# Performance work log

Measured on AMD Instinct MI355X. Metric: run time of the kernel, lower is better.

Reference implementation:

```python
import jax, jax.numpy as jnp
import numpy as np

COMBS = ((0, 1), (0, 2), (1, 2))
OUT_DIM, TIME_RANK, RANK = 3, 4, 4


def grid_sample_nd(grid, coords):
    """Multilinear interpolation. grid: [C, *R] (d spatial dims), coords: [N, d] in [-1, 1].
    align_corners=True, border clamp. Returns [N, C]."""
    d = coords.shape[-1]
    i0s, ws = [], []
    for k in range(d):
        R = grid.shape[1 + k]
        x = jnp.clip((coords[:, k] + 1.0) * 0.5 * (R - 1), 0.0, R - 1)
        i0 = jnp.clip(jnp.floor(x).astype(jnp.int32), 0, R - 2)
        i0s.append(i0)
        ws.append(x - i0)
    out = jnp.zeros((grid.shape[0], coords.shape[0]), grid.dtype)
    for corner in range(2 ** d):
        idx, w = [], jnp.ones((coords.shape[0],), grid.dtype)
        for k in range(d):
            b = (corner >> k) & 1
            idx.append(i0s[k] + b)
            w = w * (ws[k] if b else 1.0 - ws[k])
        out = out + grid[(slice(None),) + tuple(idx)] * w  # [C, N]
    return out.T


def setup_inputs():
    key = jax.random.key(0)
    ks = jax.random.split(key, 16)
    n_rays, S = 4096, 128
    N = n_rays * S
    R, T, F = 128, 150, 32
    rays_d = jax.random.normal(ks[0], (n_rays, 3), jnp.float32)
    pts = jax.random.uniform(ks[1], (N, 3), jnp.float32, -1.0, 1.0)
    times = jax.random.uniform(ks[2], (N,), jnp.float32, -1.0, 1.0)
    deltas = jax.random.uniform(ks[3], (N,), jnp.float32) * 0.02 + 1e-3
    ridx = jnp.repeat(jnp.arange(n_rays, dtype=jnp.int32), S)
    boundary = (jnp.arange(N) % S) == 0
    bg_color = jax.random.uniform(ks[4], (n_rays, 3), jnp.float32)
    grid_space = jax.random.normal(ks[5], (3, RANK * OUT_DIM * TIME_RANK, R, R), jnp.float32) * 0.1
    grid_time = jax.random.normal(ks[6], (OUT_DIM * TIME_RANK, T), jnp.float32) * 0.1
    features = jax.random.normal(ks[7], (F, R, R, R), jnp.float32) * 0.1
    W1 = jax.random.normal(ks[8], (F + 3, 64), jnp.float32) * 0.05
    b1 = jnp.zeros((64,), jnp.float32)
    W2 = jax.random.normal(ks[9], (64, 16), jnp.float32) * 0.05
    b2 = jnp.zeros((16,), jnp.float32)
    Wc1 = jax.random.normal(ks[10], (15 + 3, 64), jnp.float32) * 0.05
    bc1 = jnp.zeros((64,), jnp.float32)
    Wc2 = jax.random.normal(ks[11], (64, 3), jnp.float32) * 0.05
    bc2 = jnp.zeros((3,), jnp.float32)
    return {"rays_d": rays_d, "pts": pts, "times": times, "deltas": deltas,
            "bg_color": bg_color, "grid_space": grid_space, "grid_time": grid_time,
            "features": features, "W1": W1, "b1": b1, "W2": W2, "b2": b2,
            "Wc1": Wc1, "bc1": bc1, "Wc2": Wc2, "bc2": bc2,
            "ridx": ridx, "boundary": boundary}


def reference(rays_d, pts, times, deltas, bg_color, grid_space, grid_time, features,
              W1, b1, W2, b2, Wc1, bc1, Wc2, bc2, ridx, boundary):
    n_rays = rays_d.shape[0]
    N = pts.shape[0]
    rays_d = rays_d / jnp.linalg.norm(rays_d, axis=-1, keepdims=True)
    rd = rays_d[ridx]  # [N, 3] per-sample ray dirs

    # --- low-rank spatio-temporal feature coordinates ---
    it = grid_sample_nd(grid_time, times[:, None]).reshape(N, OUT_DIM, TIME_RANK)
    sp = jnp.stack([grid_sample_nd(grid_space[c], pts[:, list(comb)])
                    for c, comb in enumerate(COMBS)])  # [3, N, rank*out*tr]
    sp = sp.reshape(3, N, OUT_DIM, TIME_RANK, RANK)
    sp = jnp.prod(sp, axis=0).sum(axis=-1)            # [N, out_dim, time_rank]
    coords = jnp.clip((sp * it).sum(axis=-1), -1.0, 1.0)  # [N, 3]
    feats = grid_sample_nd(features, coords)          # [N, F]

    # --- MLP decoder (sigma + color) ---
    h = jax.nn.relu(jnp.concatenate([feats, rd], axis=-1) @ W1 + b1)
    s = h @ W2 + b2
    sigma = jnp.exp(jnp.clip(s[:, 0], -15.0, 15.0))   # trunc_exp
    geo = s[:, 1:]
    hc = jax.nn.relu(jnp.concatenate([geo, rd], axis=-1) @ Wc1 + bc1)
    rgb = jax.nn.sigmoid(hc @ Wc2 + bc2)              # [N, 3]

    # --- segment volumetric integration (exclusive transmittance) ---
    tau = sigma * deltas
    excl = jnp.cumsum(tau) - tau
    bmask = boundary.astype(tau.dtype)
    seg_first = jax.ops.segment_sum(excl * bmask, ridx, num_segments=n_rays)
    Tr = jnp.exp(-(excl - seg_first[ridx]))
    w = Tr * (1.0 - jnp.exp(-tau))                    # per-sample weights
    ray_colors = jax.ops.segment_sum(w[:, None] * rgb, ridx, num_segments=n_rays)
    alpha = jax.ops.segment_sum(w, ridx, num_segments=n_rays)
    return ray_colors + (1.0 - alpha)[:, None] * bg_color
```

## Files before the change

kernel.cpp:

```cpp
#include <hip/hip_runtime.h>
#include <hip/hip_fp16.h>
#include <math.h>

#define RR 128
#define TT 150
#define NCH 48
#define NF 32

typedef float vf2 __attribute__((ext_vector_type(2)));
typedef unsigned int u4v __attribute__((ext_vector_type(4)));
typedef _Float16 h2 __attribute__((ext_vector_type(2)));
typedef _Float16 h4 __attribute__((ext_vector_type(4)));
typedef float fv4 __attribute__((ext_vector_type(4)));

__device__ __forceinline__ h2 pack2(float a, float b) {
    h2 r; r[0] = (_Float16)a; r[1] = (_Float16)b; return r;
}
__device__ __forceinline__ void up4p(uint u, vf2 s, vf2* a) {
    a[0] += __builtin_amdgcn_cvt_pk_f32_fp8(u, false) * s;
    a[1] += __builtin_amdgcn_cvt_pk_f32_fp8(u, true) * s;
}
__device__ __forceinline__ void up16p(u4v q, float sf, vf2* a) {
    vf2 s; s[0] = sf; s[1] = sf;
    up4p(q[0], s, a + 0); up4p(q[1], s, a + 2);
    up4p(q[2], s, a + 4); up4p(q[3], s, a + 6);
}

__global__ __launch_bounds__(256) void tgsp_8(const float* __restrict__ in,
                                              uint* __restrict__ out) {
    __shared__ float lds[48][65];
    const int t = threadIdx.x;
    const int p = blockIdx.x >> 8;
    const int tile = blockIdx.x & 255;
    const size_t V = (size_t)RR * RR;
    const size_t v0 = (size_t)tile * 64;
    const float* ip = in + (size_t)p * NCH * V;
    uint* op = out + (size_t)p * V * 12;
    #pragma unroll
    for (int k = 0; k < 12; k++) {
        int idx = k * 256 + t; int c = idx >> 6; int vv = idx & 63;
        lds[c][vv] = ip[(size_t)c * V + v0 + vv];
    }
    __syncthreads();
    #pragma unroll
    for (int k = 0; k < 3; k++) {
        int idx = k * 256 + t; int vv = idx / 12; int cp = idx - vv * 12;
        float a = lds[4 * cp + 0][vv] * 128.f;
        float b = lds[4 * cp + 1][vv] * 128.f;
        float c = lds[4 * cp + 2][vv] * 128.f;
        float d = lds[4 * cp + 3][vv] * 128.f;
        uint w = (uint)__builtin_amdgcn_cvt_pk_fp8_f32(a, b, 0, false);
        w = (uint)__builtin_amdgcn_cvt_pk_fp8_f32(c, d, w, true);
        op[(v0 + vv) * 12 + cp] = w;
    }
}

template<bool TR>
__global__ __launch_bounds__(256, 4) void lrv_main(
    const float* __restrict__ rays_d,
    const float* __restrict__ pts,
    const float* __restrict__ times,
    const float* __restrict__ deltas,
    const float* __restrict__ bg,
    const void* __restrict__ gspace_p,
    const float* __restrict__ gtime,
    const float* __restrict__ feat,
    const float* __restrict__ W1, const float* __restrict__ b1,
    const float* __restrict__ W2, const float* __restrict__ b2,
    const float* __restrict__ Wc1, const float* __restrict__ bc1,
    const float* __restrict__ Wc2, const float* __restrict__ bc2,
    const int*  __restrict__ ridx,
    float* __restrict__ out)
{
    __shared__ __align__(16) _Float16 sW1t[64 * 48];
    __shared__ __align__(16) _Float16 sW2t[16 * 68];
    __shared__ __align__(16) _Float16 sWc1t[64 * 36];
    __shared__ __align__(16) _Float16 sWc2t[16 * 68];
    __shared__ __align__(16) _Float16 sX[4 * 64 * 48];
    __shared__ float sb1[64], sbc1[64], sb2[16], sbc2[4];
    __shared__ int sV[4], sU[4];
    __shared__ float waveTot[4];
    __shared__ float4 rbuf[4];
    float4 (*sFeatV)[8] = reinterpret_cast<float4(*)[8]>(sX);

    const int tid  = threadIdx.x;
    const int lane = tid & 63;
    const int wv   = tid >> 6;
    const int lg   = lane >> 4;
    const int ll   = lane & 15;

    {
        for (int k = tid; k < 64 * 48; k += 256) {
            int n = k / 48, kk = k - n * 48;
            sW1t[k] = (_Float16)((kk < 35) ? W1[kk * 64 + n] : 0.f);
        }
        for (int k = tid; k < 16 * 68; k += 256) {
            int o = k / 68, n = k - o * 68;
            sW2t[k] = (_Float16)((n < 64) ? W2[n * 16 + o] : 0.f);
        }
        for (int k = tid; k < 64 * 36; k += 256) {
            int n = k / 36, kk = k - n * 36;
            sWc1t[k] = (_Float16)((kk < 18) ? Wc1[kk * 64 + n] : 0.f);
        }
        for (int k = tid; k < 16 * 68; k += 256) {
            int o = k / 68, n = k - o * 68;
            sWc2t[k] = (_Float16)((o < 3 && n < 64) ? Wc2[n * 3 + o] : 0.f);
        }
        if (tid < 64) { sb1[tid] = b1[tid]; sbc1[tid] = bc1[tid]; }
        if (tid < 16) sb2[tid] = b2[tid];
        if (tid < 3)  sbc2[tid] = bc2[tid];
    }
    __syncthreads();

    const int ray = blockIdx.x * 2 + (tid >> 7);
    const int i   = ray * 128 + (tid & 127);

    float itv[12];
    {
        float t = times[i];
        float x = (t + 1.f) * 0.5f * (float)(TT - 1);
        x = fminf(fmaxf(x, 0.f), (float)(TT - 1));
        int ti0 = (int)floorf(x);
        ti0 = min(max(ti0, 0), TT - 2);
        float tw = x - (float)ti0;
        #pragma unroll
        for (int c = 0; c < 12; c++) {
            float v0 = gtime[c * TT + ti0];
            float v1 = gtime[c * TT + ti0 + 1];
            itv[c] = fmaf(tw, v1 - v0, v0);
        }
    }

    float p0 = pts[i * 3 + 0], p1 = pts[i * 3 + 1], p2 = pts[i * 3 + 2];
    int   pbia[3], pbib[3];
    float pw[3][4];
    {
        const float pa[3] = { p0, p0, p1 };
        const float pb[3] = { p1, p2, p2 };
        #pragma unroll
        for (int c = 0; c < 3; c++) {
            float xa = fminf(fmaxf((pa[c] + 1.f) * 0.5f * (float)(RR - 1), 0.f), (float)(RR - 1));
            float xb = fminf(fmaxf((pb[c] + 1.f) * 0.5f * (float)(RR - 1), 0.f), (float)(RR - 1));
            int ia = min(max((int)floorf(xa), 0), RR - 2);
            int ib = min(max((int)floorf(xb), 0), RR - 2);
            float wa = xa - (float)ia, wb = xb - (float)ib;
            pbia[c] = ia; pbib[c] = ib;
            pw[c][0] = (1.f - wa) * (1.f - wb);
            pw[c][1] = (1.f - wa) * wb;
            pw[c][2] = wa * (1.f - wb);
            pw[c][3] = wa * wb;
        }
    }
    float S12[12];
    if constexpr (TR) {
        const uint* gs = (const uint*)gspace_p;
        uint b[3][4];
        #pragma unroll
        for (int c = 0; c < 3; c++) {
            uint b00 = ((uint)c * (RR * RR) + (uint)pbia[c] * RR + (uint)pbib[c]) * 12u;
            b[c][0] = b00;            b[c][1] = b00 + 12u;
            b[c][2] = b00 + RR * 12u; b[c][3] = b00 + RR * 12u + 12u;
        }
        #pragma unroll
        for (int cb = 0; cb < 3; cb++) {
            vf2 pr[8];
            #pragma unroll
            for (int p = 0; p < 3; p++) {
                vf2 a[8];
                #pragma unroll
                for (int j = 0; j < 8; j++) { a[j][0] = 0.f; a[j][1] = 0.f; }
                #pragma unroll
                for (int corner = 0; corner < 4; corner++) {
                    u4v q = *reinterpret_cast<const u4v*>(gs + b[p][corner] + cb * 4);
                    up16p(q, pw[p][corner] * 0.0078125f, a);
                }
                #pragma unroll
                for (int j = 0; j < 8; j++) pr[j] = (p == 0) ? a[j] : pr[j] * a[j];
            }
            #pragma unroll
            for (int g = 0; g < 4; g++)
                S12[cb * 4 + g] = pr[2 * g][0] + pr[2 * g][1]
                                + pr[2 * g + 1][0] + pr[2 * g + 1][1];
        }
    } else {
        const float* gs = (const float*)gspace_p;
        #pragma unroll
        for (int k = 0; k < 12; k++) S12[k] = 0.f;
        #pragma unroll 4
        for (int ch = 0; ch < NCH; ch++) {
            float prod = 1.f;
            #pragma unroll
            for (int c = 0; c < 3; c++) {
                const float* g = gs + (size_t)(c * NCH + ch) * (RR * RR)
                               + pbia[c] * RR + pbib[c];
                float v = pw[c][0] * g[0] + pw[c][1] * g[1]
                        + pw[c][2] * g[RR] + pw[c][3] * g[RR + 1];
                prod *= v;
            }
            S12[ch >> 2] += prod;
        }
    }
    float cc[3];
    #pragma unroll
    for (int o = 0; o < 3; o++) {
        float a = 0.f;
        #pragma unroll
        for (int t = 0; t < 4; t++) a += S12[o * 4 + t] * itv[o * 4 + t];
        cc[o] = fminf(fmaxf(a, -1.f), 1.f);
    }

    __align__(16) float in35[36];
    int   fi[3];
    float cw[8];
    {
        float fw[3];
        #pragma unroll
        for (int k = 0; k < 3; k++) {
            float xk = fminf(fmaxf((cc[k] + 1.f) * 0.5f * (float)(RR - 1), 0.f), (float)(RR - 1));
            int ik = min(max((int)floorf(xk), 0), RR - 2);
            fi[k] = ik; fw[k] = xk - (float)ik;
        }
        float w0 = fw[0], w1 = fw[1], w2 = fw[2];
        cw[0] = (1.f - w0) * (1.f - w1) * (1.f - w2);
        cw[1] = (1.f - w0) * (1.f - w1) * w2;
        cw[2] = (1.f - w0) * w1 * (1.f - w2);
        cw[3] = (1.f - w0) * w1 * w2;
        cw[4] = w0 * (1.f - w1) * (1.f - w2);
        cw[5] = w0 * (1.f - w1) * w2;
        cw[6] = w0 * w1 * (1.f - w2);
        cw[7] = w0 * w1 * w2;
    }
    {
        int packed = (fi[0] << 16) | (fi[1] << 8) | fi[2];
        int first  = __builtin_amdgcn_readfirstlane(packed);
        unsigned long long bal = __ballot(packed == first);
        if (lane == 0) { sV[wv] = first; sU[wv] = (bal == ~0ull) ? 1 : 0; }
    }
    __syncthreads();
    const bool uni = sU[0] && sU[1] && sU[2] && sU[3] &&
                     sV[0] == sV[1] && sV[1] == sV[2] && sV[2] == sV[3];
    const size_t V3 = (size_t)RR * RR * RR;
    if (uni) {
        {
            int c  = tid >> 5;
            int ch = tid & 31;
            size_t off = (((size_t)(fi[0] + ((c >> 2) & 1)) * RR
                         + (size_t)(fi[1] + ((c >> 1) & 1))) * RR
                         + (size_t)(fi[2] + (c & 1)));
            ((float*)sFeatV)[c * 32 + ch] = feat[(size_t)ch * V3 + off];
        }
        __syncthreads();
        float4* in4 = reinterpret_cast<float4*>(in35);
        #pragma unroll
        for (int chq = 0; chq < 8; chq++) {
            float4 acc = make_float4(0.f, 0.f, 0.f, 0.f);
            #pragma unroll
            for (int c = 0; c < 8; c++) {
                float4 v = sFeatV[c][chq];
                acc.x = fmaf(cw[c], v.x, acc.x);
                acc.y = fmaf(cw[c], v.y, acc.y);
                acc.z = fmaf(cw[c], v.z, acc.z);
                acc.w = fmaf(cw[c], v.w, acc.w);
            }
            in4[chq] = acc;
        }
    } else {
        size_t fb = ((size_t)fi[0] * RR + fi[1]) * RR + fi[2];
        #pragma unroll 4
        for (int ch = 0; ch < NF; ch++) {
            const float* f = feat + (size_t)ch * V3 + fb;
            in35[ch] = cw[0] * f[0]            + cw[1] * f[1]
                     + cw[2] * f[RR]           + cw[3] * f[RR + 1]
                     + cw[4] * f[RR * RR]      + cw[5] * f[RR * RR + 1]
                     + cw[6] * f[RR * RR + RR] + cw[7] * f[RR * RR + RR + 1];
        }
    }
    {
        int r = ridx[i];
        float d0 = rays_d[r * 3 + 0], d1 = rays_d[r * 3 + 1], d2 = rays_d[r * 3 + 2];
        float inv = 1.f / sqrtf(d0 * d0 + d1 * d1 + d2 * d2);
        in35[32] = d0 * inv; in35[33] = d1 * inv; in35[34] = d2 * inv;
    }
    __syncthreads();

    _Float16* Xw = sX + wv * (64 * 48);
    float* Srow  = (float*)Xw;

    {
        u4v xw[6];
        #pragma unroll
        for (int t6 = 0; t6 < 6; t6++) {
            #pragma unroll
            for (int e = 0; e < 4; e++) {
                int q = t6 * 4 + e;
                float a = (2 * q     < 35) ? in35[2 * q]     : 0.f;
                float b = (2 * q + 1 < 35) ? in35[2 * q + 1] : 0.f;
                xw[t6][e] = __builtin_bit_cast(uint, pack2(a, b));
            }
        }
        u4v* xrow = (u4v*)(Xw + lane * 48);
        #pragma unroll
        for (int t6 = 0; t6 < 6; t6++) xrow[t6] = xw[t6];
    }

    fv4 bb[4];
    #pragma unroll
    for (int hr = 0; hr < 4; hr++)
        bb[hr] = *(const fv4*)&sb1[hr * 16 + (lg << 2)];
    fv4 b2v = *(const fv4*)&sb2[lg << 2];

    #pragma unroll
    for (int half = 0; half < 2; half++) {
        fv4 acc1[4][2];
        #pragma unroll
        for (int hr = 0; hr < 4; hr++) {
            acc1[hr][0] = bb[hr];
            acc1[hr][1] = bb[hr];
        }
        #pragma unroll
        for (int ks = 0; ks < 3; ks++) {
            h4 a1[4], b1f[2];
            #pragma unroll
            for (int hr = 0; hr < 4; hr++)
                a1[hr] = *(const h4*)&sW1t[(hr * 16 + ll) * 48 + ks * 16 + (lg << 2)];
            #pragma unroll
            for (int s2 = 0; s2 < 2; s2++) {
                int sc = half * 2 + s2;
                b1f[s2] = *(const h4*)&Xw[(sc * 16 + ll) * 48 + ks * 16 + (lg << 2)];
            }
            #pragma unroll
            for (int hr = 0; hr < 4; hr++) {
                acc1[hr][0] = __builtin_amdgcn_mfma_f32_16x16x16f16(a1[hr], b1f[0], acc1[hr][0], 0, 0, 0);
                acc1[hr][1] = __builtin_amdgcn_mfma_f32_16x16x16f16(a1[hr], b1f[1], acc1[hr][1], 0, 0, 0);
            }
        }
        #pragma unroll
        for (int s2 = 0; s2 < 2; s2++) {
            fv4 acc2 = b2v;
            #pragma unroll
            for (int ks = 0; ks < 4; ks++) {
                fv4 g = acc1[ks][s2];
                h4 hb;
                #pragma unroll
                for (int e = 0; e < 4; e++) hb[e] = (_Float16)fmaxf(g[e], 0.f);
                h4 a2 = *(const h4*)&sW2t[ll * 68 + ks * 16 + (lg << 2)];
                acc2 = __builtin_amdgcn_mfma_f32_16x16x16f16(a2, hb, acc2, 0, 0, 0);
            }
            int sc = half * 2 + s2;
            *(fv4*)&Srow[(sc * 16 + ll) * 20 + (lg << 2)] = acc2;
        }
    }

    float sacc[16];
    #pragma unroll
    for (int q = 0; q < 4; q++) {
        fv4 v = *(const fv4*)&Srow[lane * 20 + q * 4];
        sacc[q * 4 + 0] = v[0]; sacc[q * 4 + 1] = v[1];
        sacc[q * 4 + 2] = v[2]; sacc[q * 4 + 3] = v[3];
    }
    float sigma = __expf(fminf(fmaxf(sacc[0], -15.f), 15.f));

    {
        float xi[18];
        #pragma unroll
        for (int k = 0; k < 15; k++) xi[k] = sacc[k + 1];
        xi[15] = in35[32]; xi[16] = in35[33]; xi[17] = in35[34];
        uint wd[16];
        #pragma unroll
        for (int q = 0; q < 9; q++)
            wd[q] = __builtin_bit_cast(uint, pack2(xi[2 * q], (2 * q + 1 < 18) ? xi[2 * q + 1] : 0.f));
        #pragma unroll
        for (int q = 9; q < 16; q++) wd[q] = 0u;
        u4v* xrow = (u4v*)(Xw + lane * 48);
        #pragma unroll
        for (int t4 = 0; t4 < 4; t4++) {
            u4v v; v[0] = wd[t4 * 4 + 0]; v[1] = wd[t4 * 4 + 1];
                   v[2] = wd[t4 * 4 + 2]; v[3] = wd[t4 * 4 + 3];
            xrow[t4] = v;
        }
    }
    fv4 bbc[4];
    #pragma unroll
    for (int hr = 0; hr < 4; hr++)
        bbc[hr] = *(const fv4*)&sbc1[hr * 16 + (lg << 2)];
    fv4 c2bias;
    c2bias[0] = (lg == 0) ? sbc2[0] : 0.f;
    c2bias[1] = (lg == 0) ? sbc2[1] : 0.f;
    c2bias[2] = (lg == 0) ? sbc2[2] : 0.f;
    c2bias[3] = 0.f;

    float rc0 = 0.f, rc1 = 0.f, rc2 = 0.f;
    #pragma unroll
    for (int sc = 0; sc < 4; sc++) {
        fv4 acc1c[4];
        #pragma unroll
        for (int hr = 0; hr < 4; hr++) acc1c[hr] = bbc[hr];
        #pragma unroll
        for (int ks = 0; ks < 2; ks++) {
            h4 bfrag = *(const h4*)&Xw[(sc * 16 + ll) * 48 + ks * 16 + (lg << 2)];
            #pragma unroll
            for (int hr = 0; hr < 4; hr++) {
                h4 a = *(const h4*)&sWc1t[(hr * 16 + ll) * 36 + ks * 16 + (lg << 2)];
                acc1c[hr] = __builtin_amdgcn_mfma_f32_16x16x16f16(a, bfrag, acc1c[hr], 0, 0, 0);
            }
        }
        fv4 acc2c = c2bias;
        #pragma unroll
        for (int ks = 0; ks < 4; ks++) {
            fv4 g = acc1c[ks];
            h4 hb;
            #pragma unroll
            for (int e = 0; e < 4; e++) hb[e] = (_Float16)fmaxf(g[e], 0.f);
            h4 a2 = *(const h4*)&sWc2t[ll * 68 + ks * 16 + (lg << 2)];
            acc2c = __builtin_amdgcn_mfma_f32_16x16x16f16(a2, hb, acc2c, 0, 0, 0);
        }
        float t0 = __shfl(acc2c[0], ll, 64);
        float t1 = __shfl(acc2c[1], ll, 64);
        float t2 = __shfl(acc2c[2], ll, 64);
        if (lg == sc) { rc0 = t0; rc1 = t1; rc2 = t2; }
    }
    float r_ = 1.f / (1.f + __expf(-rc0));
    float g_ = 1.f / (1.f + __expf(-rc1));
    float b_ = 1.f / (1.f + __expf(-rc2));

    float tau = sigma * deltas[i];
    float v = tau;
    #pragma unroll
    for (int off = 1; off < 64; off <<= 1) {
        float u = __shfl_up(v, off, 64);
        if (lane >= off) v += u;
    }
    if (lane == 63) waveTot[wv] = v;
    float excl = v - tau;
    __syncthreads();
    if (wv & 1) excl += waveTot[wv & 2];

    float Tr = __expf(-excl);
    float w  = Tr * (1.f - __expf(-tau));

    float ax = w * r_, ay = w * g_, az = w * b_, aw = w;
    #pragma unroll
    for (int off = 32; off; off >>= 1) {
        ax += __shfl_down(ax, off, 64);
        ay += __shfl_down(ay, off, 64);
        az += __shfl_down(az, off, 64);
        aw += __shfl_down(aw, off, 64);
    }
    if (lane == 0) rbuf[wv] = make_float4(ax, ay, az, aw);
    __syncthreads();
    if (lane == 0 && (wv & 1) == 0) {
        float cx = rbuf[wv].x + rbuf[wv + 1].x;
        float cy = rbuf[wv].y + rbuf[wv + 1].y;
        float cz = rbuf[wv].z + rbuf[wv + 1].z;
        float alpha = rbuf[wv].w + rbuf[wv + 1].w;
        out[ray * 3 + 0] = cx + (1.f - alpha) * bg[ray * 3 + 0];
        out[ray * 3 + 1] = cy + (1.f - alpha) * bg[ray * 3 + 1];
        out[ray * 3 + 2] = cz + (1.f - alpha) * bg[ray * 3 + 2];
    }
}

extern "C" void kernel_launch(void* const* d_in, const int* in_sizes, int n_in,
                              void* d_out, int out_size, void* d_ws, size_t ws_size,
                              hipStream_t stream) {
    const float* rays_d = (const float*)d_in[0];
    const float* pts    = (const float*)d_in[1];
    const float* times  = (const float*)d_in[2];
    const float* deltas = (const float*)d_in[3];
    const float* bg     = (const float*)d_in[4];
    const float* gspace = (const float*)d_in[5];
    const float* gtime  = (const float*)d_in[6];
    const float* feat   = (const float*)d_in[7];
    const float* W1  = (const float*)d_in[8];
    const float* b1  = (const float*)d_in[9];
    const float* W2  = (const float*)d_in[10];
    const float* b2  = (const float*)d_in[11];
    const float* Wc1 = (const float*)d_in[12];
    const float* bc1 = (const float*)d_in[13];
    const float* Wc2 = (const float*)d_in[14];
    const float* bc2 = (const float*)d_in[15];
    const int*   ridx = (const int*)d_in[16];

    const int n_rays = in_sizes[0] / 3;

    const size_t GSP_8B = (size_t)3 * RR * RR * NCH;

    if (ws_size >= GSP_8B) {
        uint* gsp_t = (uint*)d_ws;
        tgsp_8<<<dim3(3 * 256), dim3(256), 0, stream>>>(gspace, gsp_t);
        lrv_main<true><<<dim3(n_rays / 2), dim3(256), 0, stream>>>(
            rays_d, pts, times, deltas, bg, (const void*)gsp_t, gtime, feat,
            W1, b1, W2, b2, Wc1, bc1, Wc2, bc2, ridx, (float*)d_out);
    } else {
        lrv_main<false><<<dim3(n_rays / 2), dim3(256), 0, stream>>>(
            rays_d, pts, times, deltas, bg, (const void*)gspace, gtime, feat,
            W1, b1, W2, b2, Wc1, bc1, Wc2, bc2, ridx, (float*)d_out);
    }
}
```

Baseline: 115.3 us.

## Halve per-wave MLP LDS staging via two-pass processing to raise occupancy

Shrinks the per-wave fp16 activation staging buffer from 64 to 32 rows. The MLP runs in two passes, with half the lanes writing their rows each pass. sFeatV gets its own small buffer instead of aliasing sX, and launch bounds rise to 5 blocks per CU. The goal is to fit more resident blocks by cutting LDS use, which hides gather latency better, at the cost of extra LDS round-trips and a tighter register budget that may cause spills.

```diff
diff --git a/kernel.cpp b/kernel.cpp
--- a/kernel.cpp
+++ b/kernel.cpp
@@ -56,7 +56,7 @@
 }
 
 template<bool TR>
-__global__ __launch_bounds__(256, 4) void lrv_main(
+__global__ __launch_bounds__(256, 5) void lrv_main(
     const float* __restrict__ rays_d,
     const float* __restrict__ pts,
     const float* __restrict__ times,
@@ -76,18 +76,20 @@
     __shared__ __align__(16) _Float16 sW2t[16 * 68];
     __shared__ __align__(16) _Float16 sWc1t[64 * 36];
     __shared__ __align__(16) _Float16 sWc2t[16 * 68];
-    __shared__ __align__(16) _Float16 sX[4 * 64 * 48];
+    __shared__ __align__(16) _Float16 sX[4 * 32 * 48];
+    __shared__ __align__(16) float4 sFeatV[8][8];
     __shared__ float sb1[64], sbc1[64], sb2[16], sbc2[4];
     __shared__ int sV[4], sU[4];
     __shared__ float waveTot[4];
     __shared__ float4 rbuf[4];
-    float4 (*sFeatV)[8] = reinterpret_cast<float4(*)[8]>(sX);
 
     const int tid  = threadIdx.x;
     const int lane = tid & 63;
     const int wv   = tid >> 6;
     const int lg   = lane >> 4;
     const int ll   = lane & 15;
+    const int myPass = lane >> 5;
+    const int mrow   = lane & 31;
 
     {
         for (int k = tid; k < 64 * 48; k += 256) {
@@ -281,27 +283,9 @@
         float inv = 1.f / sqrtf(d0 * d0 + d1 * d1 + d2 * d2);
         in35[32] = d0 * inv; in35[33] = d1 * inv; in35[34] = d2 * inv;
     }
-    __syncthreads();
-
-    _Float16* Xw = sX + wv * (64 * 48);
+
+    _Float16* Xw = sX + wv * (32 * 48);
     float* Srow  = (float*)Xw;
-
-    {
-        u4v xw[6];
-        #pragma unroll
-        for (int t6 = 0; t6 < 6; t6++) {
-            #pragma unroll
-            for (int e = 0; e < 4; e++) {
-                int q = t6 * 4 + e;
-                float a = (2 * q     < 35) ? in35[2 * q]     : 0.f;
-                float b = (2 * q + 1 < 35) ? in35[2 * q + 1] : 0.f;
-                xw[t6][e] = __builtin_bit_cast(uint, pack2(a, b));
-            }
-        }
-        u4v* xrow = (u4v*)(Xw + lane * 48);
-        #pragma unroll
-        for (int t6 = 0; t6 < 6; t6++) xrow[t6] = xw[t6];
-    }
 
     fv4 bb[4];
     #pragma unroll
@@ -309,14 +293,28 @@
         bb[hr] = *(const fv4*)&sb1[hr * 16 + (lg << 2)];
     fv4 b2v = *(const fv4*)&sb2[lg << 2];
 
-    #pragma unroll
-    for (int half = 0; half < 2; half++) {
+    float sacc[16];
+    #pragma unroll
+    for (int pass = 0; pass < 2; pass++) {
+        if (myPass == pass) {
+            u4v xw[6];
+            #pragma unroll
+            for (int t6 = 0; t6 < 6; t6++) {
+                #pragma unroll
+                for (int e = 0; e < 4; e++) {
+                    int q = t6 * 4 + e;
+                    float a = (2 * q     < 35) ? in35[2 * q]     : 0.f;
+                    float b = (2 * q + 1 < 35) ? in35[2 * q + 1] : 0.f;
+                    xw[t6][e] = __builtin_bit_cast(uint, pack2(a, b));
+                }
+            }
+            u4v* xrow = (u4v*)(Xw + mrow * 48);
+            #pragma unroll
+            for (int t6 = 0; t6 < 6; t6++) xrow[t6] = xw[t6];
+        }
         fv4 acc1[4][2];
         #pragma unroll
-        for (int hr = 0; hr < 4; hr++) {
-            acc1[hr][0] = bb[hr];
-            acc1[hr][1] = bb[hr];
-        }
+        for (int hr = 0; hr < 4; hr++) { acc1[hr][0] = bb[hr]; acc1[hr][1] = bb[hr]; }
         #pragma unroll
         for (int ks = 0; ks < 3; ks++) {
             h4 a1[4], b1f[2];
@@ -324,10 +322,8 @@
             for (int hr = 0; hr < 4; hr++)
                 a1[hr] = *(const h4*)&sW1t[(hr * 16 + ll) * 48 + ks * 16 + (lg << 2)];
             #pragma unroll
-            for (int s2 = 0; s2 < 2; s2++) {
-                int sc = half * 2 + s2;
-                b1f[s2] = *(const h4*)&Xw[(sc * 16 + ll) * 48 + ks * 16 + (lg << 2)];
-            }
+            for (int s2 = 0; s2 < 2; s2++)
+                b1f[s2] = *(const h4*)&Xw[(s2 * 16 + ll) * 48 + ks * 16 + (lg << 2)];
             #pragma unroll
             for (int hr = 0; hr < 4; hr++) {
                 acc1[hr][0] = __builtin_amdgcn_mfma_f32_16x16x16f16(a1[hr], b1f[0], acc1[hr][0], 0, 0, 0);
@@ -346,39 +342,19 @@
                 h4 a2 = *(const h4*)&sW2t[ll * 68 + ks * 16 + (lg << 2)];
                 acc2 = __builtin_amdgcn_mfma_f32_16x16x16f16(a2, hb, acc2, 0, 0, 0);
             }
-            int sc = half * 2 + s2;
-            *(fv4*)&Srow[(sc * 16 + ll) * 20 + (lg << 2)] = acc2;
-        }
-    }
-
-    float sacc[16];
-    #pragma unroll
-    for (int q = 0; q < 4; q++) {
-        fv4 v = *(const fv4*)&Srow[lane * 20 + q * 4];
-        sacc[q * 4 + 0] = v[0]; sacc[q * 4 + 1] = v[1];
-        sacc[q * 4 + 2] = v[2]; sacc[q * 4 + 3] = v[3];
+            *(fv4*)&Srow[(s2 * 16 + ll) * 20 + (lg << 2)] = acc2;
+        }
+        if (myPass == pass) {
+            #pragma unroll
+            for (int q = 0; q < 4; q++) {
+                fv4 v = *(const fv4*)&Srow[mrow * 20 + q * 4];
+                sacc[q * 4 + 0] = v[0]; sacc[q * 4 + 1] = v[1];
+                sacc[q * 4 + 2] = v[2]; sacc[q * 4 + 3] = v[3];
+            }
+        }
     }
     float sigma = __expf(fminf(fmaxf(sacc[0], -15.f), 15.f));
 
-    {
-        float xi[18];
-        #pragma unroll
-        for (int k = 0; k < 15; k++) xi[k] = sacc[k + 1];
-        xi[15] = in35[32]; xi[16] = in35[33]; xi[17] = in35[34];
-        uint wd[16];
-        #pragma unroll
-        for (int q = 0; q < 9; q++)
-            wd[q] = __builtin_bit_cast(uint, pack2(xi[2 * q], (2 * q + 1 < 18) ? xi[2 * q + 1] : 0.f));
-        #pragma unroll
-        for (int q = 9; q < 16; q++) wd[q] = 0u;
-        u4v* xrow = (u4v*)(Xw + lane * 48);
-        #pragma unroll
-        for (int t4 = 0; t4 < 4; t4++) {
-            u4v v; v[0] = wd[t4 * 4 + 0]; v[1] = wd[t4 * 4 + 1];
-                   v[2] = wd[t4 * 4 + 2]; v[3] = wd[t4 * 4 + 3];
-            xrow[t4] = v;
-        }
-    }
     fv4 bbc[4];
     #pragma unroll
     for (int hr = 0; hr < 4; hr++)
@@ -391,33 +367,55 @@
 
     float rc0 = 0.f, rc1 = 0.f, rc2 = 0.f;
     #pragma unroll
-    for (int sc = 0; sc < 4; sc++) {
-        fv4 acc1c[4];
-        #pragma unroll
-        for (int hr = 0; hr < 4; hr++) acc1c[hr] = bbc[hr];
-        #pragma unroll
-        for (int ks = 0; ks < 2; ks++) {
-            h4 bfrag = *(const h4*)&Xw[(sc * 16 + ll) * 48 + ks * 16 + (lg << 2)];
-            #pragma unroll
-            for (int hr = 0; hr < 4; hr++) {
-                h4 a = *(const h4*)&sWc1t[(hr * 16 + ll) * 36 + ks * 16 + (lg << 2)];
-                acc1c[hr] = __builtin_amdgcn_mfma_f32_16x16x16f16(a, bfrag, acc1c[hr], 0, 0, 0);
-            }
-        }
-        fv4 acc2c = c2bias;
-        #pragma unroll
-        for (int ks = 0; ks < 4; ks++) {
-            fv4 g = acc1c[ks];
-            h4 hb;
-            #pragma unroll
-            for (int e = 0; e < 4; e++) hb[e] = (_Float16)fmaxf(g[e], 0.f);
-            h4 a2 = *(const h4*)&sWc2t[ll * 68 + ks * 16 + (lg << 2)];
-            acc2c = __builtin_amdgcn_mfma_f32_16x16x16f16(a2, hb, acc2c, 0, 0, 0);
-        }
-        float t0 = __shfl(acc2c[0], ll, 64);
-        float t1 = __shfl(acc2c[1], ll, 64);
-        float t2 = __shfl(acc2c[2], ll, 64);
-        if (lg == sc) { rc0 = t0; rc1 = t1; rc2 = t2; }
+    for (int pass = 0; pass < 2; pass++) {
+        if (myPass == pass) {
+            float xi[18];
+            #pragma unroll
+            for (int k = 0; k < 15; k++) xi[k] = sacc[k + 1];
+            xi[15] = in35[32]; xi[16] = in35[33]; xi[17] = in35[34];
+            uint wd[16];
+            #pragma unroll
+            for (int q = 0; q < 9; q++)
+                wd[q] = __builtin_bit_cast(uint, pack2(xi[2 * q], (2 * q + 1 < 18) ? xi[2 * q + 1] : 0.f));
+            #pragma unroll
+            for (int q = 9; q < 16; q++) wd[q] = 0u;
+            u4v* xrow = (u4v*)(Xw + mrow * 48);
+            #pragma unroll
+            for (int t4 = 0; t4 < 4; t4++) {
+                u4v v; v[0] = wd[t4 * 4 + 0]; v[1] = wd[t4 * 4 + 1];
+                       v[2] = wd[t4 * 4 + 2]; v[3] = wd[t4 * 4 + 3];
+                xrow[t4] = v;
+            }
+        }
+        #pragma unroll
+        for (int scl = 0; scl < 2; scl++) {
+            fv4 acc1c[4];
+            #pragma unroll
+            for (int hr = 0; hr < 4; hr++) acc1c[hr] = bbc[hr];
+            #pragma unroll
+            for (int ks = 0; ks < 2; ks++) {
+                h4 bfrag = *(const h4*)&Xw[(scl * 16 + ll) * 48 + ks * 16 + (lg << 2)];
+                #pragma unroll
+                for (int hr = 0; hr < 4; hr++) {
+                    h4 a = *(const h4*)&sWc1t[(hr * 16 + ll) * 36 + ks * 16 + (lg << 2)];
+                    acc1c[hr] = __builtin_amdgcn_mfma_f32_16x16x16f16(a, bfrag, acc1c[hr], 0, 0, 0);
+                }
+            }
+            fv4 acc2c = c2bias;
+            #pragma unroll
+            for (int ks = 0; ks < 4; ks++) {
+                fv4 g = acc1c[ks];
+                h4 hb;
+                #pragma unroll
+                for (int e = 0; e < 4; e++) hb[e] = (_Float16)fmaxf(g[e], 0.f);
+                h4 a2 = *(const h4*)&sWc2t[ll * 68 + ks * 16 + (lg << 2)];
+                acc2c = __builtin_amdgcn_mfma_f32_16x16x16f16(a2, hb, acc2c, 0, 0, 0);
+            }
+            float t0 = __shfl(acc2c[0], ll, 64);
+            float t1 = __shfl(acc2c[1], ll, 64);
+            float t2 = __shfl(acc2c[2], ll, 64);
+            if (lg == pass * 2 + scl) { rc0 = t0; rc1 = t1; rc2 = t2; }
+        }
     }
     float r_ = 1.f / (1.f + __expf(-rc0));
     float g_ = 1.f / (1.f + __expf(-rc1));
```

After: 148.1 us. +28.4%, slower.
